# Performance work log

Measured on AMD Instinct MI355X. Metric: run time of the kernel, lower is better.

Reference implementation:

```python
import jax, jax.numpy as jnp
import numpy as np

N = 100000
E = 3200000
H = 4        # heads
C = 8        # hidden_dim per head
G = 512      # number of graphs
F_IN = 128
NEG_SLOPE = 0.2


def glorot(key, shape):
    fan = shape[0] + shape[-1]
    lim = jnp.sqrt(6.0 / fan)
    return jax.random.uniform(key, shape, jnp.float32, -lim, lim)


def setup_inputs() -> dict:
    key = jax.random.key(0)
    ks = jax.random.split(key, 32)
    x = jax.random.normal(ks[0], (N, F_IN), jnp.float32)
    edge_index = jax.random.randint(ks[1], (2, E), 0, N, jnp.int64)
    batch = jnp.sort(jax.random.randint(ks[2], (N,), 0, G, jnp.int64))
    d = {"x": x, "edge_index": edge_index, "batch": batch}
    in_dims = [F_IN, H * C, H * C, H * C]
    for i, din in enumerate(in_dims, start=1):
        d[f"W{i}"] = glorot(ks[3 + 4 * i], (din, H * C))
        d[f"as{i}"] = glorot(ks[4 + 4 * i], (H, C))
        d[f"ad{i}"] = glorot(ks[5 + 4 * i], (H, C))
        d[f"b{i}"] = jnp.zeros((H * C,), jnp.float32)
    d["fc_w"] = glorot(ks[30], (H * C, 1))
    d["fc_b"] = jnp.zeros((1,), jnp.float32)
    return d


def gat_layer(x, src, dst, W, a_src, a_dst, b):
    # x: [N, din]; src/dst: [E'] (with self-loops); returns [N, H*C]
    h = (x @ W).reshape(N, H, C)                         # [N,H,C]
    al_s = jnp.einsum('nhc,hc->nh', h, a_src)            # [N,H]
    al_d = jnp.einsum('nhc,hc->nh', h, a_dst)
    e = jax.nn.leaky_relu(al_s[src] + al_d[dst], NEG_SLOPE)  # [E',H]
    m = jax.ops.segment_max(e, dst, num_segments=N)      # [N,H]
    ee = jnp.exp(e - m[dst])
    denom = jax.ops.segment_sum(ee, dst, num_segments=N) # [N,H]
    alpha = ee / denom[dst]
    msg = alpha[:, :, None] * h[src]                     # [E',H,C]
    out = jax.ops.segment_sum(msg, dst, num_segments=N)  # [N,H,C]
    return out.reshape(N, H * C) + b


def reference(x, edge_index, batch, W1, as1, ad1, b1, W2, as2, ad2, b2,
              W3, as3, ad3, b3, W4, as4, ad4, b4, fc_w, fc_b):
    # PyG GATConv default: add self-loops
    loop = jnp.arange(N, dtype=edge_index.dtype)
    src = jnp.concatenate([edge_index[0], loop])
    dst = jnp.concatenate([edge_index[1], loop])
    h = jax.nn.elu(gat_layer(x, src, dst, W1, as1, ad1, b1))
    h = jax.nn.elu(gat_layer(h, src, dst, W2, as2, ad2, b2))
    h = jax.nn.elu(gat_layer(h, src, dst, W3, as3, ad3, b3))
    h = jax.nn.elu(gat_layer(h, src, dst, W4, as4, ad4, b4))
    # global mean pool over graphs
    sums = jax.ops.segment_sum(h, batch, num_segments=G)          # [G,HC]
    cnts = jax.ops.segment_sum(jnp.ones((N,), h.dtype), batch, num_segments=G)
    pooled = sums / jnp.maximum(cnts, 1.0)[:, None]
    return pooled @ fc_w + fc_b                                   # [G,1]
```

## Files before the change

kernel.cpp:

```cpp
#include <hip/hip_runtime.h>
#include <hip/hip_fp16.h>
#include <math.h>

#define NN 100000
#define NE 3200000
#define NHEAD 4
#define HC 32
#define NG 512
#define EDGES (NE + NN)

#define G1BLKS (NN / 8)

#define BKT_BITS 9
#define BKT_SIZE 512
#define NBKT 196
#define CHUNK1 16384
#define NB1 ((EDGES + CHUNK1 - 1) / CHUNK1)
#define NB1S 204
#define CAP2 18432
#define PCHUNK 128

__device__ __forceinline__ float lrelu(float x) { return x > 0.f ? x : 0.2f * x; }

__global__ __launch_bounds__(256) void gemm1_hist(
    const float* __restrict__ x, const float* __restrict__ W1,
    const float* __restrict__ as1, const float* __restrict__ ad1,
    __half* __restrict__ h, float* __restrict__ als, float* __restrict__ ald,
    const int* __restrict__ ei, int* __restrict__ CmatT) {
    __shared__ float Wl[128 * HC];
    __shared__ float xl[8][128];
    __shared__ int hcnt[NBKT];
    int tid = threadIdx.x;
    if (blockIdx.x >= G1BLKS) {
        int b1 = blockIdx.x - G1BLKS;
        for (int i = tid; i < NBKT; i += 256) hcnt[i] = 0;
        __syncthreads();
        int base = b1 * CHUNK1;
        int lim = min(base + CHUNK1, EDGES);
        for (int e = base + tid; e < lim; e += 256) {
            int dst = (e < NE) ? ei[NE + e] : (e - NE);
            atomicAdd(&hcnt[dst >> BKT_BITS], 1);
        }
        __syncthreads();
        for (int i = tid; i < NBKT; i += 256)
            CmatT[i * NB1S + b1] = hcnt[i];
        return;
    }
    for (int i = tid; i < 128 * HC; i += 256) Wl[i] = W1[i];
    int n0 = blockIdx.x * 8;
    {
        float4 v = *reinterpret_cast<const float4*>(x + n0 * 128 + tid * 4);
        int idx = tid * 4;
        int r = idx >> 7, c = idx & 127;
        *reinterpret_cast<float4*>(&xl[r][c]) = v;
    }
    __syncthreads();
    int r = tid >> 5, col = tid & 31;
    int n = n0 + r;
    float acc = 0.f;
#pragma unroll
    for (int k = 0; k < 128; ++k) acc = fmaf(xl[r][k], Wl[k * HC + col], acc);
    float s = acc * as1[col];
    float d = acc * ad1[col];
#pragma unroll
    for (int off = 1; off < 8; off <<= 1) {
        s += __shfl_xor(s, off);
        d += __shfl_xor(d, off);
    }
    h[n * HC + col] = __float2half(acc);
    if ((col & 7) == 0) {
        als[n * NHEAD + (col >> 3)] = s;
        ald[n * NHEAD + (col >> 3)] = d;
    }
}

__global__ __launch_bounds__(64) void colscan2(int* __restrict__ CmatT,
                                               int* __restrict__ degTot) {
    int k = blockIdx.x;
    int lane = threadIdx.x;
    int* p = CmatT + k * NB1S;
    int i0 = lane * 4;
    int v0 = (i0 + 0 < NB1) ? p[i0 + 0] : 0;
    int v1 = (i0 + 1 < NB1) ? p[i0 + 1] : 0;
    int v2 = (i0 + 2 < NB1) ? p[i0 + 2] : 0;
    int v3 = (i0 + 3 < NB1) ? p[i0 + 3] : 0;
    int e1 = v0, e2 = v0 + v1, e3 = v0 + v1 + v2;
    int tot = e3 + v3;
    int run = tot;
#pragma unroll
    for (int off = 1; off < 64; off <<= 1) {
        int u = __shfl_up(run, off);
        if (lane >= off) run += u;
    }
    int excl = run - tot;
    if (i0 + 0 < NB1) p[i0 + 0] = excl;
    if (i0 + 1 < NB1) p[i0 + 1] = excl + e1;
    if (i0 + 2 < NB1) p[i0 + 2] = excl + e2;
    if (i0 + 3 < NB1) p[i0 + 3] = excl + e3;
    if (lane == 63) degTot[k] = run;
}

__global__ __launch_bounds__(256) void bucket_apex(const int* __restrict__ degTot,
                                                   int* __restrict__ bucketStart) {
    __shared__ int tot[256];
    int k = threadIdx.x;
    int own = (k < NBKT) ? degTot[k] : 0;
    tot[k] = own;
    __syncthreads();
    for (int off = 1; off < 256; off <<= 1) {
        int u = (k >= off) ? tot[k - off] : 0;
        __syncthreads();
        tot[k] += u;
        __syncthreads();
    }
    if (k < NBKT) bucketStart[k] = tot[k] - own;
    if (k == 255) bucketStart[NBKT] = tot[255];
}

__global__ __launch_bounds__(512) void pass1_scatter(const int* __restrict__ ei,
                                                     const int* __restrict__ CmatT,
                                                     const int* __restrict__ bucketStart,
                                                     unsigned int* __restrict__ ebuf) {
    __shared__ int cur[NBKT];
    for (int i = threadIdx.x; i < NBKT; i += 512)
        cur[i] = bucketStart[i] + CmatT[i * NB1S + blockIdx.x];
    __syncthreads();
    int base = blockIdx.x * CHUNK1;
    int lim = min(base + CHUNK1, EDGES);
    for (int e = base + threadIdx.x; e < lim; e += 512) {
        int src, dst;
        if (e < NE) { src = ei[e]; dst = ei[NE + e]; }
        else        { src = dst = e - NE; }
        int pos = atomicAdd(&cur[dst >> BKT_BITS], 1);
        ebuf[pos] = ((unsigned int)(dst & (BKT_SIZE - 1)) << 20) | (unsigned int)src;
    }
}

__global__ __launch_bounds__(1024) void pass2_sort(const unsigned int* __restrict__ ebuf,
                                                   const int* __restrict__ bucketStart,
                                                   int* __restrict__ csrsrc,
                                                   int* __restrict__ rowst) {
    __shared__ int hist[BKT_SIZE];
    __shared__ int scn[BKT_SIZE];
    __shared__ int staging[CAP2];
    int t = threadIdx.x;
    int k = blockIdx.x;
    int start = bucketStart[k], end = bucketStart[k + 1];
    int count = end - start;
    if (t < BKT_SIZE) hist[t] = 0;
    __syncthreads();
    for (int i = start + t; i < end; i += 1024)
        atomicAdd(&hist[ebuf[i] >> 20], 1);
    __syncthreads();
    if (t < BKT_SIZE) scn[t] = hist[t];
    __syncthreads();
    for (int off = 1; off < BKT_SIZE; off <<= 1) {
        int u = (t < BKT_SIZE && t >= off) ? scn[t - off] : 0;
        __syncthreads();
        if (t < BKT_SIZE) scn[t] += u;
        __syncthreads();
    }
    if (t < BKT_SIZE) {
        int ex = scn[t] - hist[t];
        rowst[k * BKT_SIZE + t] = start + ex;
        hist[t] = ex;
    }
    __syncthreads();
    for (int i = start + t; i < end; i += 1024) {
        unsigned int v = ebuf[i];
        int pos = atomicAdd(&hist[v >> 20], 1);
        if (pos < CAP2) staging[pos] = (int)(v & 0xFFFFFu);
    }
    __syncthreads();
    for (int i = t; i < count; i += 1024) csrsrc[start + i] = staging[i];
}

template<bool FUSE>
__global__ __launch_bounds__(256) void agg_layer(
    const int* __restrict__ rowst, const int* __restrict__ csrsrc,
    const float* __restrict__ als, const float* __restrict__ ald,
    const __half* __restrict__ h, const float* __restrict__ bias,
    const float* __restrict__ Wn, const float* __restrict__ asn,
    const float* __restrict__ adn,
    __half* __restrict__ h_out, float* __restrict__ als_out,
    float* __restrict__ ald_out, float* __restrict__ act_out) {
    __shared__ float Wl[HC * HC];
    int tid = threadIdx.x;
    if (FUSE) {
        for (int i = tid; i < HC * HC; i += 256) Wl[i] = Wn[i];
        __syncthreads();
    }
    int g = blockIdx.x * 8 + (tid >> 5);
    int lane = tid & 31;
    int head = lane >> 3;
    int slot = lane & 7;
    float adh = ald[g * NHEAD + head];
    int beg = rowst[g], end = rowst[g + 1];

    float acc[8];
#pragma unroll
    for (int j = 0; j < 8; ++j) acc[j] = 0.f;
    float dsum = 0.f;
    const __half* hL = h + lane;

    int e0 = beg + slot;
    int sP = (e0 < end) ? __builtin_nontemporal_load(csrsrc + e0) : 0;
    float aP = als[sP * NHEAD + head];

    for (int c0 = beg; c0 < end; c0 += 8) {
        int eN = c0 + 8 + slot;
        int sN = (eN < end) ? __builtin_nontemporal_load(csrsrc + eN) : 0;
        float aN = als[sN * NHEAD + head];
        bool ok = (c0 + slot) < end;
        float p = __expf(lrelu(aP + adh));
        p = ok ? p : 0.f;
        dsum += p;
#pragma unroll
        for (int j = 0; j < 8; ++j) {
            float pj = __shfl(p, (head << 3) | j, 32);
            int sj = __shfl(sP, j, 32);
            acc[j] = fmaf(pj, __half2float(hL[sj * HC]), acc[j]);
        }
        sP = sN;
        aP = aN;
    }
    float a = ((acc[0] + acc[1]) + (acc[2] + acc[3])) +
              ((acc[4] + acc[5]) + (acc[6] + acc[7]));
    dsum += __shfl_xor(dsum, 1, 32);
    dsum += __shfl_xor(dsum, 2, 32);
    dsum += __shfl_xor(dsum, 4, 32);

    float v = a / dsum + bias[lane];
    float av = v > 0.f ? v : (__expf(v) - 1.f);
    if (!FUSE) {
        act_out[g * HC + lane] = av;
        return;
    }
    float hacc = 0.f;
#pragma unroll
    for (int kk = 0; kk < HC; ++kk)
        hacc = fmaf(__shfl(av, kk, 32), Wl[kk * HC + lane], hacc);
    h_out[g * HC + lane] = __float2half(hacc);
    float sv = hacc * asn[lane];
    float dv = hacc * adn[lane];
#pragma unroll
    for (int off = 1; off < 8; off <<= 1) {
        sv += __shfl_xor(sv, off);
        dv += __shfl_xor(dv, off);
    }
    if ((lane & 7) == 0) {
        als_out[g * NHEAD + head] = sv;
        ald_out[g * NHEAD + head] = dv;
    }
}

__global__ void pool_init(float* __restrict__ sums, float* __restrict__ cnt) {
    int i = blockIdx.x * blockDim.x + threadIdx.x;
    if (i < NG * HC) sums[i] = 0.f;
    if (i < NG) cnt[i] = 0.f;
}

__global__ __launch_bounds__(256) void pool_seg(const float* __restrict__ act,
                                                const int* __restrict__ batch,
                                                float* __restrict__ sums,
                                                float* __restrict__ cnt) {
    int grp = blockIdx.x * 8 + (threadIdx.x >> 5);
    int lane = threadIdx.x & 31;
    int n0 = grp * PCHUNK;
    if (n0 >= NN) return;
    int n1 = min(n0 + PCHUNK, NN);
    int curg = batch[n0];
    float acc = 0.f, c = 0.f;
    for (int n = n0; n < n1; ++n) {
        int gg = batch[n];
        if (gg != curg) {
            atomicAdd(&sums[curg * HC + lane], acc);
            if (lane == 0) atomicAdd(&cnt[curg], c);
            acc = 0.f; c = 0.f; curg = gg;
        }
        acc += act[n * HC + lane];
        c += 1.f;
    }
    atomicAdd(&sums[curg * HC + lane], acc);
    if (lane == 0) atomicAdd(&cnt[curg], c);
}

__global__ void fc_out(const float* __restrict__ sums, const float* __restrict__ cnt,
                       const float* __restrict__ fcw, const float* __restrict__ fcb,
                       float* __restrict__ out) {
    int g = blockIdx.x;
    int lane = threadIdx.x;
    float v = (lane < HC) ? sums[g * HC + lane] * fcw[lane] : 0.f;
#pragma unroll
    for (int off = 32; off; off >>= 1) v += __shfl_down(v, off);
    if (lane == 0) out[g] = v / fmaxf(cnt[g], 1.f) + fcb[0];
}

extern "C" void kernel_launch(void* const* d_in, const int* in_sizes, int n_in,
                              void* d_out, int out_size, void* d_ws, size_t ws_size,
                              hipStream_t stream) {
    const float* x     = (const float*)d_in[0];
    const int*   ei    = (const int*)d_in[1];
    const int*   batch = (const int*)d_in[2];
    const float* W[4]   = {(const float*)d_in[3],  (const float*)d_in[7],
                           (const float*)d_in[11], (const float*)d_in[15]};
    const float* asr[4] = {(const float*)d_in[4],  (const float*)d_in[8],
                           (const float*)d_in[12], (const float*)d_in[16]};
    const float* adt[4] = {(const float*)d_in[5],  (const float*)d_in[9],
                           (const float*)d_in[13], (const float*)d_in[17]};
    const float* bb[4]  = {(const float*)d_in[6],  (const float*)d_in[10],
                           (const float*)d_in[14], (const float*)d_in[18]};
    const float* fcw = (const float*)d_in[19];
    const float* fcb = (const float*)d_in[20];
    float* out = (float*)d_out;

    char* ws = (char*)d_ws;
    size_t off = 0;
    auto carve = [&](size_t bytes) {
        void* p = ws + off;
        off += (bytes + 255) & ~size_t(255);
        return p;
    };
    __half* hA   = (__half*)carve(sizeof(__half) * NN * HC);
    __half* hB   = (__half*)carve(sizeof(__half) * NN * HC);
    float* actF  = (float*)carve(sizeof(float) * NN * HC);
    float* alsA  = (float*)carve(sizeof(float) * NN * NHEAD);
    float* aldA  = (float*)carve(sizeof(float) * NN * NHEAD);
    float* alsB  = (float*)carve(sizeof(float) * NN * NHEAD);
    float* aldB  = (float*)carve(sizeof(float) * NN * NHEAD);
    int*   CmatT = (int*)carve(sizeof(int) * NBKT * NB1S);
    int*   degTot= (int*)carve(sizeof(int) * NBKT);
    int*   bkst  = (int*)carve(sizeof(int) * (NBKT + 1));
    unsigned int* ebuf = (unsigned int*)carve(sizeof(unsigned int) * EDGES);
    int*   rowst = (int*)carve(sizeof(int) * NBKT * BKT_SIZE);
    int*   csrsrc= (int*)carve(sizeof(int) * EDGES);
    float* sums  = (float*)carve(sizeof(float) * NG * HC);
    float* cnt   = (float*)carve(sizeof(float) * NG);

    gemm1_hist<<<G1BLKS + NB1, 256, 0, stream>>>(x, W[0], asr[0], adt[0],
                                                 hA, alsA, aldA, ei, CmatT);
    colscan2<<<NBKT, 64, 0, stream>>>(CmatT, degTot);
    bucket_apex<<<1, 256, 0, stream>>>(degTot, bkst);
    pass1_scatter<<<NB1, 512, 0, stream>>>(ei, CmatT, bkst, ebuf);
    pass2_sort<<<NBKT, 1024, 0, stream>>>(ebuf, bkst, csrsrc, rowst);

    agg_layer<true><<<G1BLKS, 256, 0, stream>>>(rowst, csrsrc, alsA, aldA, hA, bb[0],
                                                W[1], asr[1], adt[1],
                                                hB, alsB, aldB, nullptr);
    agg_layer<true><<<G1BLKS, 256, 0, stream>>>(rowst, csrsrc, alsB, aldB, hB, bb[1],
                                                W[2], asr[2], adt[2],
                                                hA, alsA, aldA, nullptr);
    agg_layer<true><<<G1BLKS, 256, 0, stream>>>(rowst, csrsrc, alsA, aldA, hA, bb[2],
                                                W[3], asr[3], adt[3],
                                                hB, alsB, aldB, nullptr);
    agg_layer<false><<<G1BLKS, 256, 0, stream>>>(rowst, csrsrc, alsB, aldB, hB, bb[3],
                                                 nullptr, nullptr, nullptr,
                                                 nullptr, nullptr, nullptr, actF);

    pool_init<<<(NG * HC + 255) / 256, 256, 0, stream>>>(sums, cnt);
    pool_seg<<<((NN + PCHUNK - 1) / PCHUNK + 7) / 8, 256, 0, stream>>>(actF, batch,
                                                                       sums, cnt);
    fc_out<<<NG, 64, 0, stream>>>(sums, cnt, fcw, fcb, out);
}
```

Baseline: 461.7 us.

## Split node features into two half-width arrays and aggregate per half

Node features are stored as two separate 16-channel fp16 arrays (heads 0-1 and heads 2-3), and each layer's aggregation runs as two passes, one per half. The idea is that each pass gathers from a 3.2 MB table instead of 6.4 MB, which should keep the random gathers in cache. The next-layer GEMM that used to be fused into aggregation now runs as its own kernel and reads an fp32 activation buffer. In exchange, the CSR indices and attention scores are read twice per layer, the software prefetch of the next edge's index is gone, and extra kernel launches and activation traffic are added.

```diff
diff --git a/kernel.cpp b/kernel.cpp
--- a/kernel.cpp
+++ b/kernel.cpp
@@ -25,7 +25,8 @@
 __global__ __launch_bounds__(256) void gemm1_hist(
     const float* __restrict__ x, const float* __restrict__ W1,
     const float* __restrict__ as1, const float* __restrict__ ad1,
-    __half* __restrict__ h, float* __restrict__ als, float* __restrict__ ald,
+    __half* __restrict__ hLo, __half* __restrict__ hHi,
+    float* __restrict__ als, float* __restrict__ ald,
     const int* __restrict__ ei, int* __restrict__ CmatT) {
     __shared__ float Wl[128 * HC];
     __shared__ float xl[8][128];
@@ -67,7 +68,8 @@
         s += __shfl_xor(s, off);
         d += __shfl_xor(d, off);
     }
-    h[n * HC + col] = __float2half(acc);
+    if (col < 16) hLo[n * 16 + col] = __float2half(acc);
+    else          hHi[n * 16 + col - 16] = __float2half(acc);
     if ((col & 7) == 0) {
         als[n * NHEAD + (col >> 3)] = s;
         ald[n * NHEAD + (col >> 3)] = d;
@@ -175,82 +177,84 @@
     for (int i = t; i < count; i += 1024) csrsrc[start + i] = staging[i];
 }
 
-template<bool FUSE>
-__global__ __launch_bounds__(256) void agg_layer(
+template<int HALF, bool LAST>
+__global__ __launch_bounds__(256) void agg_half(
     const int* __restrict__ rowst, const int* __restrict__ csrsrc,
     const float* __restrict__ als, const float* __restrict__ ald,
-    const __half* __restrict__ h, const float* __restrict__ bias,
-    const float* __restrict__ Wn, const float* __restrict__ asn,
-    const float* __restrict__ adn,
-    __half* __restrict__ h_out, float* __restrict__ als_out,
-    float* __restrict__ ald_out, float* __restrict__ act_out) {
-    __shared__ float Wl[HC * HC];
+    const __half* __restrict__ hH, const float* __restrict__ bias,
+    float* __restrict__ actOut) {
     int tid = threadIdx.x;
-    if (FUSE) {
-        for (int i = tid; i < HC * HC; i += 256) Wl[i] = Wn[i];
-        __syncthreads();
-    }
     int g = blockIdx.x * 8 + (tid >> 5);
     int lane = tid & 31;
     int head = lane >> 3;
     int slot = lane & 7;
+    int ch = lane & 15;
+    int pair = lane >> 4;
     float adh = ald[g * NHEAD + head];
     int beg = rowst[g], end = rowst[g + 1];
 
-    float acc[8];
-#pragma unroll
-    for (int j = 0; j < 8; ++j) acc[j] = 0.f;
+    float acc[4] = {0.f, 0.f, 0.f, 0.f};
     float dsum = 0.f;
-    const __half* hL = h + lane;
-
-    int e0 = beg + slot;
-    int sP = (e0 < end) ? __builtin_nontemporal_load(csrsrc + e0) : 0;
-    float aP = als[sP * NHEAD + head];
+    const __half* hC = hH + ch;
+    int hd = HALF * 2 + (ch >> 3);
+    int psrc = hd << 3;
 
     for (int c0 = beg; c0 < end; c0 += 8) {
-        int eN = c0 + 8 + slot;
-        int sN = (eN < end) ? __builtin_nontemporal_load(csrsrc + eN) : 0;
-        float aN = als[sN * NHEAD + head];
-        bool ok = (c0 + slot) < end;
-        float p = __expf(lrelu(aP + adh));
+        int e = c0 + slot;
+        bool ok = (e < end);
+        int s = ok ? __builtin_nontemporal_load(csrsrc + e) : 0;
+        float p = __expf(lrelu(als[s * NHEAD + head] + adh));
         p = ok ? p : 0.f;
         dsum += p;
 #pragma unroll
-        for (int j = 0; j < 8; ++j) {
-            float pj = __shfl(p, (head << 3) | j, 32);
-            int sj = __shfl(sP, j, 32);
-            acc[j] = fmaf(pj, __half2float(hL[sj * HC]), acc[j]);
+        for (int i = 0; i < 4; ++i) {
+            int em = 2 * i + pair;
+            int sm = __shfl(s, em, 32);
+            float pm = __shfl(p, psrc | em, 32);
+            acc[i] = fmaf(pm, __half2float(hC[sm * 16]), acc[i]);
         }
-        sP = sN;
-        aP = aN;
-    }
-    float a = ((acc[0] + acc[1]) + (acc[2] + acc[3])) +
-              ((acc[4] + acc[5]) + (acc[6] + acc[7]));
+    }
+    float a = (acc[0] + acc[1]) + (acc[2] + acc[3]);
+    a += __shfl_xor(a, 16, 32);
     dsum += __shfl_xor(dsum, 1, 32);
     dsum += __shfl_xor(dsum, 2, 32);
     dsum += __shfl_xor(dsum, 4, 32);
-
-    float v = a / dsum + bias[lane];
+    float dm = __shfl(dsum, psrc, 32);
+
+    float v = a / dm + bias[HALF * 16 + ch];
     float av = v > 0.f ? v : (__expf(v) - 1.f);
-    if (!FUSE) {
-        act_out[g * HC + lane] = av;
-        return;
-    }
+    if (pair == 0)
+        actOut[g * HC + HALF * 16 + ch] = av;
+}
+
+__global__ __launch_bounds__(256) void gemm32(
+    const float* __restrict__ actU, const float* __restrict__ Wn,
+    const float* __restrict__ asn, const float* __restrict__ adn,
+    __half* __restrict__ hLo, __half* __restrict__ hHi,
+    float* __restrict__ als, float* __restrict__ ald) {
+    __shared__ float Wl[HC * HC];
+    int tid = threadIdx.x;
+    for (int i = tid; i < HC * HC; i += 256) Wl[i] = Wn[i];
+    __syncthreads();
+    int n = blockIdx.x * 8 + (tid >> 5);
+    int col = tid & 31;
+    float av = actU[n * HC + col];
     float hacc = 0.f;
 #pragma unroll
-    for (int kk = 0; kk < HC; ++kk)
-        hacc = fmaf(__shfl(av, kk, 32), Wl[kk * HC + lane], hacc);
-    h_out[g * HC + lane] = __float2half(hacc);
-    float sv = hacc * asn[lane];
-    float dv = hacc * adn[lane];
+    for (int k = 0; k < HC; ++k)
+        hacc = fmaf(__shfl(av, k, 32), Wl[k * HC + col], hacc);
+    if (col < 16) hLo[n * 16 + col] = __float2half(hacc);
+    else          hHi[n * 16 + col - 16] = __float2half(hacc);
+    float sv = hacc * asn[col];
+    float dv = hacc * adn[col];
 #pragma unroll
     for (int off = 1; off < 8; off <<= 1) {
         sv += __shfl_xor(sv, off);
         dv += __shfl_xor(dv, off);
     }
-    if ((lane & 7) == 0) {
-        als_out[g * NHEAD + head] = sv;
-        ald_out[g * NHEAD + head] = dv;
+    if ((col & 7) == 0) {
+        als[n * NHEAD + (col >> 3)] = sv;
+        ald[n * NHEAD + (col >> 3)] = dv;
     }
 }
 
@@ -321,13 +325,12 @@
         off += (bytes + 255) & ~size_t(255);
         return p;
     };
-    __half* hA   = (__half*)carve(sizeof(__half) * NN * HC);
-    __half* hB   = (__half*)carve(sizeof(__half) * NN * HC);
+    __half* hLo  = (__half*)carve(sizeof(__half) * NN * 16);
+    __half* hHi  = (__half*)carve(sizeof(__half) * NN * 16);
+    float* actU  = (float*)carve(sizeof(float) * NN * HC);
     float* actF  = (float*)carve(sizeof(float) * NN * HC);
-    float* alsA  = (float*)carve(sizeof(float) * NN * NHEAD);
-    float* aldA  = (float*)carve(sizeof(float) * NN * NHEAD);
-    float* alsB  = (float*)carve(sizeof(float) * NN * NHEAD);
-    float* aldB  = (float*)carve(sizeof(float) * NN * NHEAD);
+    float* als   = (float*)carve(sizeof(float) * NN * NHEAD);
+    float* ald   = (float*)carve(sizeof(float) * NN * NHEAD);
     int*   CmatT = (int*)carve(sizeof(int) * NBKT * NB1S);
     int*   degTot= (int*)carve(sizeof(int) * NBKT);
     int*   bkst  = (int*)carve(sizeof(int) * (NBKT + 1));
@@ -338,24 +341,27 @@
     float* cnt   = (float*)carve(sizeof(float) * NG);
 
     gemm1_hist<<<G1BLKS + NB1, 256, 0, stream>>>(x, W[0], asr[0], adt[0],
-                                                 hA, alsA, aldA, ei, CmatT);
+                                                 hLo, hHi, als, ald, ei, CmatT);
     colscan2<<<NBKT, 64, 0, stream>>>(CmatT, degTot);
     bucket_apex<<<1, 256, 0, stream>>>(degTot, bkst);
     pass1_scatter<<<NB1, 512, 0, stream>>>(ei, CmatT, bkst, ebuf);
     pass2_sort<<<NBKT, 1024, 0, stream>>>(ebuf, bkst, csrsrc, rowst);
 
-    agg_layer<true><<<G1BLKS, 256, 0, stream>>>(rowst, csrsrc, alsA, aldA, hA, bb[0],
-                                                W[1], asr[1], adt[1],
-                                                hB, alsB, aldB, nullptr);
-    agg_layer<true><<<G1BLKS, 256, 0, stream>>>(rowst, csrsrc, alsB, aldB, hB, bb[1],
-                                                W[2], asr[2], adt[2],
-                                                hA, alsA, aldA, nullptr);
-    agg_layer<true><<<G1BLKS, 256, 0, stream>>>(rowst, csrsrc, alsA, aldA, hA, bb[2],
-                                                W[3], asr[3], adt[3],
-                                                hB, alsB, aldB, nullptr);
-    agg_layer<false><<<G1BLKS, 256, 0, stream>>>(rowst, csrsrc, alsB, aldB, hB, bb[3],
-                                                 nullptr, nullptr, nullptr,
-                                                 nullptr, nullptr, nullptr, actF);
+    for (int L = 0; L < 4; ++L) {
+        if (L < 3) {
+            agg_half<0, false><<<G1BLKS, 256, 0, stream>>>(rowst, csrsrc, als, ald,
+                                                           hLo, bb[L], actU);
+            agg_half<1, false><<<G1BLKS, 256, 0, stream>>>(rowst, csrsrc, als, ald,
+                                                           hHi, bb[L], actU);
+            gemm32<<<G1BLKS, 256, 0, stream>>>(actU, W[L + 1], asr[L + 1], adt[L + 1],
+                                               hLo, hHi, als, ald);
+        } else {
+            agg_half<0, true><<<G1BLKS, 256, 0, stream>>>(rowst, csrsrc, als, ald,
+                                                          hLo, bb[3], actF);
+            agg_half<1, true><<<G1BLKS, 256, 0, stream>>>(rowst, csrsrc, als, ald,
+                                                          hHi, bb[3], actF);
+        }
+    }
 
     pool_init<<<(NG * HC + 255) / 256, 256, 0, stream>>>(sums, cnt);
     pool_seg<<<((NN + PCHUNK - 1) / PCHUNK + 7) / 8, 256, 0, stream>>>(actF, batch,
```

Result: slower. 717.4 us (+55.4%).
